# Optimization experiments

Measured on AMD Instinct MI355X. Metric: run time of the kernel, lower is better.

The kernel has to match this reference:

```python
import jax, jax.numpy as jnp
import numpy as np

N_NODES = 100000

def _gcn_layer(x, W, b, src, dst, n):
    # x: [N, Fin], W: [Fin, Fout], b: [Fout]; edges src->dst, [E]
    h = x @ W  # [N, Fout]
    # add self loops
    loops = jnp.arange(n, dtype=src.dtype)
    s = jnp.concatenate([src, loops])
    d = jnp.concatenate([dst, loops])
    # symmetric GCN normalization: deg^{-1/2}[s] * deg^{-1/2}[d]
    deg = jax.ops.segment_sum(jnp.ones_like(d, dtype=h.dtype), d, num_segments=n)
    dis = jnp.where(deg > 0, jax.lax.rsqrt(jnp.maximum(deg, 1.0)), 0.0)
    norm = dis[s] * dis[d]  # [E+N]
    msg = h[s] * norm[:, None]  # [E+N, Fout]
    out = jax.ops.segment_sum(msg, d, num_segments=n)  # [N, Fout]
    return out + b


def setup_inputs() -> dict:
    key = jax.random.key(0)
    k1, k2, k3, k4, k5 = jax.random.split(key, 5)
    in_feat, hidden, out_feat = 64, 128, 64
    n_edges = 1600000
    node_features = jax.random.normal(k1, (N_NODES, in_feat), dtype=jnp.float32)
    edge_index = jax.random.randint(k2, (2, n_edges), 0, N_NODES, dtype=jnp.int32)
    # glorot-ish params
    W1 = jax.random.normal(k3, (in_feat, hidden), dtype=jnp.float32) * (1.0 / np.sqrt(in_feat))
    b1 = jnp.zeros((hidden,), dtype=jnp.float32)
    W2 = jax.random.normal(k4, (hidden, out_feat), dtype=jnp.float32) * (1.0 / np.sqrt(hidden))
    b2 = jnp.zeros((out_feat,), dtype=jnp.float32)
    return {"node_features": node_features, "edge_index": edge_index,
            "W1": W1, "b1": b1, "W2": W2, "b2": b2}


def reference(node_features, edge_index, W1, b1, W2, b2):
    src, dst = edge_index[0], edge_index[1]
    n = node_features.shape[0]
    h = _gcn_layer(node_features, W1, b1, src, dst, n)
    h = jax.nn.relu(h)
    h = _gcn_layer(h, W2, b2, src, dst, n)
    return h
```

## Files before the change

kernel.cpp:

```cpp
#include <hip/hip_runtime.h>
#include <hip/hip_fp16.h>

#define NN 100000
#define NB 391
#define NG 256
#define SCAN_B 256

using f16x8 = __attribute__((ext_vector_type(8))) _Float16;
using f32x4 = __attribute__((ext_vector_type(4))) float;

__global__ __launch_bounds__(256) void bhist_kernel(const int* __restrict__ dst,
                                                    int* __restrict__ counts, int E) {
    __shared__ int h[NB];
    for (int i = threadIdx.x; i < NB; i += 256) h[i] = 0;
    __syncthreads();
    const int chunk = (E + NG - 1) / NG;
    const int lo = blockIdx.x * chunk, hi = min(E, lo + chunk);
    for (int e = lo + threadIdx.x; e < hi; e += 256) atomicAdd(&h[dst[e] >> 8], 1);
    __syncthreads();
    for (int i = threadIdx.x; i < NB; i += 256) counts[i * NG + blockIdx.x] = h[i];
}

__global__ void scan1_kernel(int* __restrict__ a, int* __restrict__ blk_sums, int M) {
    __shared__ int sm[SCAN_B];
    int t = threadIdx.x, i = blockIdx.x * SCAN_B + t;
    int v = (i < M) ? a[i] : 0;
    sm[t] = v; __syncthreads();
    for (int off = 1; off < SCAN_B; off <<= 1) {
        int x = (t >= off) ? sm[t - off] : 0; __syncthreads();
        sm[t] += x; __syncthreads();
    }
    if (i < M) a[i] = sm[t] - v;
    if (t == SCAN_B - 1) blk_sums[blockIdx.x] = sm[t];
}

__global__ void scan2_kernel(const int* __restrict__ blk_sums, int* __restrict__ blk_off, int nblk) {
    __shared__ int sm[SCAN_B];
    __shared__ int run;
    int t = threadIdx.x;
    if (t == 0) run = 0;
    __syncthreads();
    for (int base = 0; base < nblk; base += SCAN_B) {
        int i = base + t;
        int v = (i < nblk) ? blk_sums[i] : 0;
        sm[t] = v; __syncthreads();
        for (int off = 1; off < SCAN_B; off <<= 1) {
            int x = (t >= off) ? sm[t - off] : 0; __syncthreads();
            sm[t] += x; __syncthreads();
        }
        if (i < nblk) blk_off[i] = run + sm[t] - v;
        __syncthreads();
        if (t == 0) run += sm[SCAN_B - 1];
        __syncthreads();
    }
}

__global__ void scan3_kernel(int* __restrict__ a, const int* __restrict__ blk_off, int M) {
    int i = blockIdx.x * SCAN_B + threadIdx.x;
    if (i < M) a[i] += blk_off[blockIdx.x];
}

__global__ __launch_bounds__(256) void bscatter_kernel(const int* __restrict__ src,
                                                       const int* __restrict__ dst,
                                                       const int* __restrict__ cstart,
                                                       int* __restrict__ staging, int E) {
    __shared__ int cur[NB];
    for (int i = threadIdx.x; i < NB; i += 256) cur[i] = cstart[i * NG + blockIdx.x];
    __syncthreads();
    const int chunk = (E + NG - 1) / NG;
    const int lo = blockIdx.x * chunk, hi = min(E, lo + chunk);
    for (int e = lo + threadIdx.x; e < hi; e += 256) {
        int d = dst[e];
        int pos = atomicAdd(&cur[d >> 8], 1);
        staging[pos] = src[e] | ((d & 255) << 17);
    }
}

__global__ __launch_bounds__(256) void bfinal_kernel(const int* __restrict__ cstart,
                                                     const int* __restrict__ staging,
                                                     int* __restrict__ csr_src,
                                                     int* __restrict__ row_start,
                                                     float* __restrict__ dis, int N, int E) {
    __shared__ int h[256];
    __shared__ int sc[256];
    __shared__ int cur[256];
    const int b = blockIdx.x, t = threadIdx.x;
    const int base = cstart[b * NG];
    const int endb = (b == NB - 1) ? E : cstart[(b + 1) * NG];
    h[t] = 0; __syncthreads();
    for (int i = base + t; i < endb; i += 256) atomicAdd(&h[staging[i] >> 17], 1);
    __syncthreads();
    int v = h[t];
    sc[t] = v; __syncthreads();
    for (int off = 1; off < 256; off <<= 1) {
        int x = (t >= off) ? sc[t - off] : 0; __syncthreads();
        sc[t] += x; __syncthreads();
    }
    int excl = sc[t] - v;
    cur[t] = base + excl;
    int node = b * 256 + t;
    if (node < N) {
        row_start[node] = base + excl;
        dis[node] = rsqrtf((float)v + 1.0f);
    }
    if (b == NB - 1 && t == 0) row_start[N] = E;
    __syncthreads();
    for (int i = base + t; i < endb; i += 256) {
        int p = staging[i];
        int pos = atomicAdd(&cur[p >> 17], 1);
        csr_src[pos] = p & 0x1FFFF;
    }
}

__global__ void cvt_kernel(const float* __restrict__ in, const float* __restrict__ dis,
                           __half* __restrict__ out, long long n4) {
    long long i = (long long)blockIdx.x * blockDim.x + threadIdx.x;
    if (i >= n4) return;
    float4 v = ((const float4*)in)[i];
    float w = dis[(int)(i >> 4)];
    __half2* o = (__half2*)out;
    o[2 * i]     = __floats2half2_rn(v.x * w, v.y * w);
    o[2 * i + 1] = __floats2half2_rn(v.z * w, v.w * w);
}

template<int K, int F>
__global__ void cvtWt_kernel(const float* __restrict__ W, __half* __restrict__ Wt) {
    int i = blockIdx.x * 256 + threadIdx.x;
    if (i >= K * F) return;
    int k = i / F, c = i % F;
    Wt[c * K + k] = __float2half(W[i]);
}

template<int K, int F, int EPI>
__global__ __launch_bounds__(256) void gemm_mfma_kernel(const __half* __restrict__ A,
                                                        const __half* __restrict__ Wt,
                                                        const float* __restrict__ bias,
                                                        const float* __restrict__ dis,
                                                        __half* __restrict__ C, int N) {
    constexpr int BM = 32;
    constexpr int NT = F / 32;
    const int wid  = threadIdx.x >> 6;
    const int lane = threadIdx.x & 63;
    const int wr = wid >> 1;
    const int wc = wid & 1;
    const int row0 = blockIdx.x * BM + wr * 16;
    const int col0 = wc * (F / 2);
    const int lrow = lane & 15;
    const int kgrp = lane >> 4;

    f32x4 acc[NT];
    #pragma unroll
    for (int nt = 0; nt < NT; ++nt) acc[nt] = (f32x4){0.f, 0.f, 0.f, 0.f};

    #pragma unroll
    for (int ks = 0; ks < K / 32; ++ks) {
        const int kbase = ks * 32 + kgrp * 8;
        f16x8 a = *reinterpret_cast<const f16x8*>(&A[(size_t)(row0 + lrow) * K + kbase]);
        #pragma unroll
        for (int nt = 0; nt < NT; ++nt) {
            f16x8 b = *reinterpret_cast<const f16x8*>(&Wt[(size_t)(col0 + nt * 16 + lrow) * K + kbase]);
            acc[nt] = __builtin_amdgcn_mfma_f32_16x16x32_f16(a, b, acc[nt], 0, 0, 0);
        }
    }
    #pragma unroll
    for (int nt = 0; nt < NT; ++nt) {
        const int col = col0 + nt * 16 + lrow;
        float bb = (EPI == 0) ? bias[col] : 0.0f;
        #pragma unroll
        for (int r = 0; r < 4; ++r) {
            const int row = row0 + kgrp * 4 + r;
            float v = acc[nt][r];
            if (EPI == 0) v = fmaxf(v + bb, 0.0f);
            else          v = v * dis[row];
            C[(size_t)row * F + col] = __float2half(v);
        }
    }
}

template<bool BIAS, typename OutT>
__global__ __launch_bounds__(256) void gather64v2_kernel(const __half* __restrict__ tab,
                                                         const float* __restrict__ dis,
                                                         const float* __restrict__ b,
                                                         const int* __restrict__ row_start,
                                                         const int* __restrict__ csr_src,
                                                         OutT* __restrict__ out, int N) {
    const int node = blockIdx.x * 4 + (threadIdx.x >> 6);
    const int lane = threadIdx.x & 63;
    const int g   = lane >> 3;
    const int sub = lane & 7;
    if (node >= N) return;
    const int beg = row_start[node], end = row_start[node + 1];

    float acc[8];
    {
        f16x8 sv = *reinterpret_cast<const f16x8*>(&tab[(size_t)node * 64 + sub * 8]);
        #pragma unroll
        for (int q = 0; q < 8; ++q) acc[q] = (g == 0) ? (float)sv[q] : 0.0f;
    }

    int j = beg;
    #pragma unroll 2
    for (; j + 8 <= end; j += 8) {
        int s = csr_src[j + g];
        f16x8 v = *reinterpret_cast<const f16x8*>(&tab[(size_t)s * 64 + sub * 8]);
        #pragma unroll
        for (int q = 0; q < 8; ++q) acc[q] += (float)v[q];
    }
    if (j + g < end) {
        int s = csr_src[j + g];
        f16x8 v = *reinterpret_cast<const f16x8*>(&tab[(size_t)s * 64 + sub * 8]);
        #pragma unroll
        for (int q = 0; q < 8; ++q) acc[q] += (float)v[q];
    }

    #pragma unroll
    for (int q = 0; q < 8; ++q) {
        acc[q] += __shfl_xor(acc[q], 8);
        acc[q] += __shfl_xor(acc[q], 16);
        acc[q] += __shfl_xor(acc[q], 32);
    }

    if (g == 0) {
        const float dd = dis[node];
        if constexpr (sizeof(OutT) == 2) {
            f16x8 o;
            #pragma unroll
            for (int q = 0; q < 8; ++q) {
                float v = acc[q] * dd;
                if (BIAS) v += b[sub * 8 + q];
                o[q] = (_Float16)v;
            }
            *reinterpret_cast<f16x8*>(&out[(size_t)node * 64 + sub * 8]) = o;
        } else {
            float4 o0, o1;
            float vv[8];
            #pragma unroll
            for (int q = 0; q < 8; ++q) {
                float v = acc[q] * dd;
                if (BIAS) v += b[sub * 8 + q];
                vv[q] = v;
            }
            o0 = make_float4(vv[0], vv[1], vv[2], vv[3]);
            o1 = make_float4(vv[4], vv[5], vv[6], vv[7]);
            float* op = (float*)&out[(size_t)node * 64 + sub * 8];
            *reinterpret_cast<float4*>(op)     = o0;
            *reinterpret_cast<float4*>(op + 4) = o1;
        }
    }
}

extern "C" void kernel_launch(void* const* d_in, const int* in_sizes, int n_in,
                              void* d_out, int out_size, void* d_ws, size_t ws_size,
                              hipStream_t stream) {
    const float* x  = (const float*)d_in[0];
    const int*   ei = (const int*)d_in[1];
    const float* W1 = (const float*)d_in[2];
    const float* b1 = (const float*)d_in[3];
    const float* W2 = (const float*)d_in[4];
    const float* b2 = (const float*)d_in[5];
    float* out = (float*)d_out;

    const int N = NN;
    const int E = in_sizes[1] / 2;
    const int* src = ei;
    const int* dst = ei + E;
    const int M = NB * NG;
    const int scan_blocks = (M + SCAN_B - 1) / SCAN_B;

    int* counts    = (int*)d_ws;
    int* blk_sums  = counts + M;
    int* blk_off   = blk_sums + 1024;
    int* row_start = blk_off + 1024;
    float* dis     = (float*)(row_start + N + 64);
    int* staging   = (int*)(dis + N);
    int* csr_src   = staging + E;
    float* base    = (float*)(csr_src + E);
    __half* xh     = (__half*)base;
    __half* aggh   = (__half*)(base + (size_t)N * 32);
    __half* zh     = (__half*)(base + (size_t)N * 64);
    __half* h1h    = (__half*)(base + (size_t)N * 96);
    __half* W1t    = (__half*)(base + (size_t)N * 160);
    __half* W2t    = W1t + 128 * 64;

    bhist_kernel<<<NG, 256, 0, stream>>>(dst, counts, E);
    scan1_kernel<<<scan_blocks, SCAN_B, 0, stream>>>(counts, blk_sums, M);
    scan2_kernel<<<1, SCAN_B, 0, stream>>>(blk_sums, blk_off, scan_blocks);
    scan3_kernel<<<scan_blocks, SCAN_B, 0, stream>>>(counts, blk_off, M);
    bscatter_kernel<<<NG, 256, 0, stream>>>(src, dst, counts, staging, E);
    bfinal_kernel<<<NB, 256, 0, stream>>>(counts, staging, csr_src, row_start, dis, N, E);

    cvtWt_kernel<64, 128><<<(64 * 128 + 255) / 256, 256, 0, stream>>>(W1, W1t);
    cvtWt_kernel<128, 64><<<(128 * 64 + 255) / 256, 256, 0, stream>>>(W2, W2t);

    {
        long long n4 = (long long)N * 64 / 4;
        cvt_kernel<<<(int)((n4 + 255) / 256), 256, 0, stream>>>(x, dis, xh, n4);
    }
    gather64v2_kernel<false, __half><<<(N + 3) / 4, 256, 0, stream>>>(xh, dis, nullptr, row_start, csr_src, aggh, N);
    gemm_mfma_kernel<64, 128, 0><<<N / 32, 256, 0, stream>>>(aggh, W1t, b1, nullptr, h1h, N);

    gemm_mfma_kernel<128, 64, 1><<<N / 32, 256, 0, stream>>>(h1h, W2t, nullptr, dis, zh, N);
    gather64v2_kernel<true, float><<<(N + 3) / 4, 256, 0, stream>>>(zh, dis, b2, row_start, csr_src, out, N);
}
```

Baseline: 191.9 us.

## Fuse feature conversion into CSR finalize and double gather loads per iteration

```diff
diff --git a/kernel.cpp b/kernel.cpp
--- a/kernel.cpp
+++ b/kernel.cpp
@@ -80,10 +80,14 @@
                                                      const int* __restrict__ staging,
                                                      int* __restrict__ csr_src,
                                                      int* __restrict__ row_start,
-                                                     float* __restrict__ dis, int N, int E) {
+                                                     float* __restrict__ dis,
+                                                     const float* __restrict__ x,
+                                                     __half* __restrict__ xh,
+                                                     int N, int E) {
     __shared__ int h[256];
     __shared__ int sc[256];
     __shared__ int cur[256];
+    __shared__ float sdis[256];
     const int b = blockIdx.x, t = threadIdx.x;
     const int base = cstart[b * NG];
     const int endb = (b == NB - 1) ? E : cstart[(b + 1) * NG];
@@ -93,15 +97,17 @@
     int v = h[t];
     sc[t] = v; __syncthreads();
     for (int off = 1; off < 256; off <<= 1) {
-        int x = (t >= off) ? sc[t - off] : 0; __syncthreads();
-        sc[t] += x; __syncthreads();
+        int xv = (t >= off) ? sc[t - off] : 0; __syncthreads();
+        sc[t] += xv; __syncthreads();
     }
     int excl = sc[t] - v;
     cur[t] = base + excl;
+    float dv = rsqrtf((float)v + 1.0f);
+    sdis[t] = dv;
     int node = b * 256 + t;
     if (node < N) {
         row_start[node] = base + excl;
-        dis[node] = rsqrtf((float)v + 1.0f);
+        dis[node] = dv;
     }
     if (b == NB - 1 && t == 0) row_start[N] = E;
     __syncthreads();
@@ -110,17 +116,16 @@
         int pos = atomicAdd(&cur[p >> 17], 1);
         csr_src[pos] = p & 0x1FFFF;
     }
-}
-
-__global__ void cvt_kernel(const float* __restrict__ in, const float* __restrict__ dis,
-                           __half* __restrict__ out, long long n4) {
-    long long i = (long long)blockIdx.x * blockDim.x + threadIdx.x;
-    if (i >= n4) return;
-    float4 v = ((const float4*)in)[i];
-    float w = dis[(int)(i >> 4)];
-    __half2* o = (__half2*)out;
-    o[2 * i]     = __floats2half2_rn(v.x * w, v.y * w);
-    o[2 * i + 1] = __floats2half2_rn(v.z * w, v.w * w);
+    const int node0 = b * 256;
+    const int nmax = min(256, N - node0);
+    for (int i = t; i < nmax * 16; i += 256) {
+        int nl = i >> 4, c4 = i & 15;
+        float4 vx = ((const float4*)x)[((size_t)(node0 + nl) * 64 + c4 * 4) >> 2];
+        float w = sdis[nl];
+        __half2* o = (__half2*)&xh[(size_t)(node0 + nl) * 64 + c4 * 4];
+        o[0] = __floats2half2_rn(vx.x * w, vx.y * w);
+        o[1] = __floats2half2_rn(vx.z * w, vx.w * w);
+    }
 }
 
 template<int K, int F>
@@ -178,12 +183,13 @@
 }
 
 template<bool BIAS, typename OutT>
-__global__ __launch_bounds__(256) void gather64v2_kernel(const __half* __restrict__ tab,
+__global__ __launch_bounds__(256) void gather64v3_kernel(const __half* __restrict__ tab,
                                                          const float* __restrict__ dis,
                                                          const float* __restrict__ b,
                                                          const int* __restrict__ row_start,
                                                          const int* __restrict__ csr_src,
-                                                         OutT* __restrict__ out, int N) {
+                                                         OutT* __restrict__ out, int N,
+                                                         float one) {
     const int node = blockIdx.x * 4 + (threadIdx.x >> 6);
     const int lane = threadIdx.x & 63;
     const int g   = lane >> 3;
@@ -199,18 +205,28 @@
     }
 
     int j = beg;
-    #pragma unroll 2
-    for (; j + 8 <= end; j += 8) {
+    for (; j + 16 <= end; j += 16) {
+        int sA = csr_src[j + g];
+        int sB = csr_src[j + 8 + g];
+        f16x8 vA = *reinterpret_cast<const f16x8*>(&tab[(size_t)sA * 64 + sub * 8]);
+        f16x8 vB = *reinterpret_cast<const f16x8*>(&tab[(size_t)sB * 64 + sub * 8]);
+        #pragma unroll
+        for (int q = 0; q < 8; ++q) acc[q] = fmaf((float)vA[q], one, acc[q]);
+        #pragma unroll
+        for (int q = 0; q < 8; ++q) acc[q] = fmaf((float)vB[q], one, acc[q]);
+    }
+    if (j + 8 <= end) {
         int s = csr_src[j + g];
         f16x8 v = *reinterpret_cast<const f16x8*>(&tab[(size_t)s * 64 + sub * 8]);
         #pragma unroll
-        for (int q = 0; q < 8; ++q) acc[q] += (float)v[q];
+        for (int q = 0; q < 8; ++q) acc[q] = fmaf((float)v[q], one, acc[q]);
+        j += 8;
     }
     if (j + g < end) {
         int s = csr_src[j + g];
         f16x8 v = *reinterpret_cast<const f16x8*>(&tab[(size_t)s * 64 + sub * 8]);
         #pragma unroll
-        for (int q = 0; q < 8; ++q) acc[q] += (float)v[q];
+        for (int q = 0; q < 8; ++q) acc[q] = fmaf((float)v[q], one, acc[q]);
     }
 
     #pragma unroll
@@ -232,7 +248,6 @@
             }
             *reinterpret_cast<f16x8*>(&out[(size_t)node * 64 + sub * 8]) = o;
         } else {
-            float4 o0, o1;
             float vv[8];
             #pragma unroll
             for (int q = 0; q < 8; ++q) {
@@ -240,11 +255,9 @@
                 if (BIAS) v += b[sub * 8 + q];
                 vv[q] = v;
             }
-            o0 = make_float4(vv[0], vv[1], vv[2], vv[3]);
-            o1 = make_float4(vv[4], vv[5], vv[6], vv[7]);
             float* op = (float*)&out[(size_t)node * 64 + sub * 8];
-            *reinterpret_cast<float4*>(op)     = o0;
-            *reinterpret_cast<float4*>(op + 4) = o1;
+            *reinterpret_cast<float4*>(op)     = make_float4(vv[0], vv[1], vv[2], vv[3]);
+            *reinterpret_cast<float4*>(op + 4) = make_float4(vv[4], vv[5], vv[6], vv[7]);
         }
     }
 }
@@ -287,18 +300,14 @@
     scan2_kernel<<<1, SCAN_B, 0, stream>>>(blk_sums, blk_off, scan_blocks);
     scan3_kernel<<<scan_blocks, SCAN_B, 0, stream>>>(counts, blk_off, M);
     bscatter_kernel<<<NG, 256, 0, stream>>>(src, dst, counts, staging, E);
-    bfinal_kernel<<<NB, 256, 0, stream>>>(counts, staging, csr_src, row_start, dis, N, E);
+    bfinal_kernel<<<NB, 256, 0, stream>>>(counts, staging, csr_src, row_start, dis, x, xh, N, E);
 
     cvtWt_kernel<64, 128><<<(64 * 128 + 255) / 256, 256, 0, stream>>>(W1, W1t);
     cvtWt_kernel<128, 64><<<(128 * 64 + 255) / 256, 256, 0, stream>>>(W2, W2t);
 
-    {
-        long long n4 = (long long)N * 64 / 4;
-        cvt_kernel<<<(int)((n4 + 255) / 256), 256, 0, stream>>>(x, dis, xh, n4);
-    }
-    gather64v2_kernel<false, __half><<<(N + 3) / 4, 256, 0, stream>>>(xh, dis, nullptr, row_start, csr_src, aggh, N);
+    gather64v3_kernel<false, __half><<<(N + 3) / 4, 256, 0, stream>>>(xh, dis, nullptr, row_start, csr_src, aggh, N, 1.0f);
     gemm_mfma_kernel<64, 128, 0><<<N / 32, 256, 0, stream>>>(aggh, W1t, b1, nullptr, h1h, N);
 
     gemm_mfma_kernel<128, 64, 1><<<N / 32, 256, 0, stream>>>(h1h, W2t, nullptr, dis, zh, N);
-    gather64v2_kernel<true, float><<<(N + 3) / 4, 256, 0, stream>>>(zh, dis, b2, row_start, csr_src, out, N);
-}
+    gather64v3_kernel<true, float><<<(N + 3) / 4, 256, 0, stream>>>(zh, dis, b2, row_start, csr_src, out, N, 1.0f);
+}
```

New measurement: 189.4 us. No clear change (-1.3%).
